# Kernel tuning notes

Measured on AMD Instinct MI355X. Metric: run time of the kernel, lower is better.

Reference implementation:

```python
import jax, jax.numpy as jnp
import numpy as np

DIM_MODEL = 512
KDIM = 64
NUM_FREQS = 70


def setup_inputs() -> dict:
    key = jax.random.key(0)
    ks = jax.random.split(key, 8)
    B, N = 8, 2048
    src = jax.random.normal(ks[0], (B, N, DIM_MODEL), dtype=jnp.float32)
    bias_tensor = jax.random.normal(ks[1], (N, N, 4), dtype=jnp.float32)
    multiplier = jax.random.uniform(ks[2], (B, N, N), dtype=jnp.float32)
    # f_theta_lc params
    W_r = jax.random.normal(ks[3], (NUM_FREQS, 2), dtype=jnp.float32)  # std=1.0 init
    C = jnp.ones((NUM_FREQS,), dtype=jnp.float32)
    log_p = jnp.float32(0.0)
    # Xavier-uniform attention projections (torch Linear weight layout [out, in])
    lim = float(np.sqrt(6.0 / (DIM_MODEL + KDIM)))
    W_q = jax.random.uniform(ks[4], (KDIM, DIM_MODEL), minval=-lim, maxval=lim, dtype=jnp.float32)
    W_k = jax.random.uniform(ks[5], (KDIM, DIM_MODEL), minval=-lim, maxval=lim, dtype=jnp.float32)
    W_v = jax.random.uniform(ks[6], (KDIM, DIM_MODEL), minval=-lim, maxval=lim, dtype=jnp.float32)
    s = jnp.float32(1.0)
    return {"src": src, "bias_tensor": bias_tensor, "multiplier": multiplier,
            "W_r": W_r, "C": C, "log_p": log_p,
            "W_q": W_q, "W_k": W_k, "W_v": W_v, "s": s}


def _f_theta(bias_tensor, W_r, C, log_p):
    # bias_tensor: [N, N, 4]; W_r: [F, 2]
    k1 = jnp.einsum('nmi,fi->nmf', bias_tensor[:, :, 0:2], W_r)
    k2 = jnp.einsum('nmi,fi->nmf', bias_tensor[:, :, 2:4], W_r)
    diff = jnp.cos(k1) + jnp.sin(k1) - jnp.cos(k2) - jnp.sin(k2)
    sigma = jnp.abs(jnp.sum(diff * C, axis=-1))  # [N, N]
    p = jnp.clip(jnp.exp(log_p), 0.5, 3.0)
    return jnp.exp(-jnp.power(sigma + 1e-6, p))


def reference(src, bias_tensor, multiplier, W_r, C, log_p, W_q, W_k, W_v, s):
    B = _f_theta(bias_tensor, W_r, C, log_p)  # [N, N]
    Q = jnp.einsum('bnd,kd->bnk', src, W_q)
    K = jnp.einsum('bnd,kd->bnk', src, W_k)
    V = jnp.einsum('bnd,kd->bnk', src, W_v)
    denom = jnp.sqrt(jnp.float32(KDIM))
    logits = (jnp.einsum('bnk,bmk->bnm', Q, K) + B[None]) / denom
    logits = logits * (s * multiplier)
    attn = jax.nn.softmax(logits, axis=-1)
    return jnp.einsum('bnm,bmk->bnk', attn, V)
```

## Files before the change

### kernel.cpp

```cpp
#include <hip/hip_runtime.h>
#include <hip/hip_bf16.h>

#define N_SEQ 2048
#define NB 8
#define DM 512
#define KD 64
#define NF 70

#define TG 512
#define TRANGE 6.5f
#define TSCL (511.0f / 13.0f)
#define TOFS (6.5f * TSCL)

typedef float f32x4 __attribute__((ext_vector_type(4)));
typedef short v8s  __attribute__((ext_vector_type(8)));

__device__ __forceinline__ ushort f2bf(float x) {
    uint u = __float_as_uint(x);
    return (ushort)((u + 0x7FFFu + ((u >> 16) & 1u)) >> 16);
}
__device__ __forceinline__ float bf2f(ushort h) {
    return __uint_as_float(((uint)h) << 16);
}

__global__ __launch_bounds__(256) void tbuild_kernel(
    const float* __restrict__ Wr, const float* __restrict__ Cc,
    float* __restrict__ Tg)
{
    const float SQ2 = 1.41421356237309504880f;
    const float R2PI = 0.15915494309189533577f;
    int idx = blockIdx.x * 256 + threadIdx.x;
    int j = idx >> 9, i = idx & (TG - 1);
    const float h = 2.0f * TRANGE / (TG - 1);
    float y = -TRANGE + j * h;
    float x = -TRANGE + i * h;
    float g = 0.f;
    for (int f = 0; f < NF; ++f) {
        float w0 = Wr[2*f] * R2PI, w1 = Wr[2*f+1] * R2PI, cf = Cc[f];
        float k = __builtin_amdgcn_fractf(fmaf(x, w0, fmaf(y, w1, 0.125f)));
        g = fmaf(cf, __builtin_amdgcn_sinf(k), g);
    }
    Tg[idx] = g * SQ2;
}

__global__ __launch_bounds__(256) void tpack_kernel(
    const float* __restrict__ Tg, float4* __restrict__ T4)
{
    int idx = blockIdx.x * 256 + threadIdx.x;
    int j = idx >> 9, i = idx & (TG - 1);
    int i1 = min(i + 1, TG - 1);
    int j1 = min(j + 1, TG - 1);
    float4 q;
    q.x = Tg[j*TG + i];
    q.y = Tg[j*TG + i1];
    q.z = Tg[j1*TG + i];
    q.w = Tg[j1*TG + i1];
    T4[idx] = q;
}

__device__ __forceinline__ float tlookup(const float4* __restrict__ T4,
                                         float x, float y)
{
    float u = fmaf(x, TSCL, TOFS);
    float v = fmaf(y, TSCL, TOFS);
    u = fminf(fmaxf(u, 0.0f), 510.999f);
    v = fminf(fmaxf(v, 0.0f), 510.999f);
    int iu = (int)u, iv = (int)v;
    float fu = __builtin_amdgcn_fractf(u);
    float fv = __builtin_amdgcn_fractf(v);
    float4 q = T4[iv * TG + iu];
    float t0 = fmaf(fu, q.y - q.x, q.x);
    float t1 = fmaf(fu, q.w - q.z, q.z);
    return fmaf(fv, t1 - t0, t0);
}

__global__ __launch_bounds__(256) void ftheta_kernel(
    const float* __restrict__ bias, const float4* __restrict__ T4,
    const float* __restrict__ logp, ushort* __restrict__ Bm)
{
    int tid = threadIdx.x;
    long i0 = (long)blockIdx.x * 512 + tid;
    long i1 = i0 + 256;
    float4 a = ((const float4*)bias)[i0];
    float4 b = ((const float4*)bias)[i1];
    float gA1 = tlookup(T4, a.x, a.y);
    float gA2 = tlookup(T4, a.z, a.w);
    float gB1 = tlookup(T4, b.x, b.y);
    float gB2 = tlookup(T4, b.z, b.w);
    float s0 = fabsf(gA1 - gA2) + 1e-6f;
    float s1 = fabsf(gB1 - gB2) + 1e-6f;
    float p = __expf(logp[0]);
    p = fminf(fmaxf(p, 0.5f), 3.0f);
    if (p == 1.0f) {
        Bm[i0] = f2bf(__expf(-s0));
        Bm[i1] = f2bf(__expf(-s1));
    } else {
        Bm[i0] = f2bf(__expf(-__powf(s0, p)));
        Bm[i1] = f2bf(__expf(-__powf(s1, p)));
    }
}

__global__ __launch_bounds__(256) void qkv_kernel(
    const float* __restrict__ src, const float* __restrict__ Wq,
    const float* __restrict__ Wk, const float* __restrict__ Wv,
    ushort* __restrict__ Qh, ushort* __restrict__ Ql,
    ushort* __restrict__ Kh, ushort* __restrict__ VhT)
{
    __shared__ ushort sS[32][72];
    __shared__ ushort sW[192][72];
    int tid = threadIdx.x;
    int lane = tid & 63, w = tid >> 6;
    int wr = w >> 1, wc = w & 1;
    int g = lane >> 4, ln = lane & 15;
    int row0 = blockIdx.x * 32;

    f32x4 acc[6];
#pragma unroll
    for (int t = 0; t < 6; ++t) acc[t] = {0.f, 0.f, 0.f, 0.f};

    for (int kc = 0; kc < 8; ++kc) {
        int k0 = kc * 64;
        __syncthreads();
        {
            int r = tid >> 3, c8 = (tid & 7) * 8;
            float4 f0 = *(const float4*)&src[(long)(row0 + r)*DM + k0 + c8];
            float4 f1 = *(const float4*)&src[(long)(row0 + r)*DM + k0 + c8 + 4];
            *(ushort4*)&sS[r][c8] =
                make_ushort4(f2bf(f0.x), f2bf(f0.y), f2bf(f0.z), f2bf(f0.w));
            *(ushort4*)&sS[r][c8+4] =
                make_ushort4(f2bf(f1.x), f2bf(f1.y), f2bf(f1.z), f2bf(f1.w));
        }
        {
#pragma unroll
            for (int j = 0; j < 6; ++j) {
                int slot = tid + j*256;
                int r = slot >> 3, c8 = (slot & 7) * 8;
                const float* Wp = (r < 64) ? Wq : (r < 128 ? Wk : Wv);
                int rr = r & 63;
                float4 f0 = *(const float4*)&Wp[(long)rr*DM + k0 + c8];
                float4 f1 = *(const float4*)&Wp[(long)rr*DM + k0 + c8 + 4];
                *(ushort4*)&sW[r][c8] =
                    make_ushort4(f2bf(f0.x), f2bf(f0.y), f2bf(f0.z), f2bf(f0.w));
                *(ushort4*)&sW[r][c8+4] =
                    make_ushort4(f2bf(f1.x), f2bf(f1.y), f2bf(f1.z), f2bf(f1.w));
            }
        }
        __syncthreads();
#pragma unroll
        for (int kw = 0; kw < 2; ++kw) {
            v8s bsrc = *(const v8s*)&sS[16*wr + ln][32*kw + 8*g];
#pragma unroll
            for (int t = 0; t < 6; ++t) {
                v8s aw = *(const v8s*)&sW[96*wc + 16*t + ln][32*kw + 8*g];
                acc[t] = __builtin_amdgcn_mfma_f32_16x16x32_bf16(aw, bsrc, acc[t], 0, 0, 0);
            }
        }
    }
    int n = row0 + 16*wr + ln;
    int bb = n >> 11, nn = n & 2047;
#pragma unroll
    for (int t = 0; t < 6; ++t) {
        int c0 = 96*wc + 16*t + 4*g;
        f32x4 v = acc[t];
        ushort4 h = make_ushort4(f2bf(v[0]), f2bf(v[1]), f2bf(v[2]), f2bf(v[3]));
        if (c0 < 64) {
            *(ushort4*)&Qh[(long)n*KD + c0] = h;
            *(ushort4*)&Ql[(long)n*KD + c0] =
                make_ushort4(f2bf(v[0] - bf2f(h.x)), f2bf(v[1] - bf2f(h.y)),
                             f2bf(v[2] - bf2f(h.z)), f2bf(v[3] - bf2f(h.w)));
        } else if (c0 < 128) {
            *(ushort4*)&Kh[(long)n*KD + (c0 - 64)] = h;
        } else {
            int kv = c0 - 128;
            VhT[((long)bb*KD + kv + 0)*N_SEQ + nn] = h.x;
            VhT[((long)bb*KD + kv + 1)*N_SEQ + nn] = h.y;
            VhT[((long)bb*KD + kv + 2)*N_SEQ + nn] = h.z;
            VhT[((long)bb*KD + kv + 3)*N_SEQ + nn] = h.w;
        }
    }
}

__global__ __launch_bounds__(256, 4) void attn_mfma_kernel(
    const ushort* __restrict__ Qh, const ushort* __restrict__ Ql,
    const ushort* __restrict__ Kh, const ushort* __restrict__ VhT,
    const ushort* __restrict__ Bm, const float* __restrict__ mult,
    const float* __restrict__ sp,
    ushort* __restrict__ Opart, float* __restrict__ Mp, float* __restrict__ Lp)
{
    __shared__ ushort sKh[64][72];
    __shared__ ushort sVT[64][72];
    __shared__ ushort sP[4][16][72];

    int tid = threadIdx.x;
    int lane = tid & 63, w = tid >> 6;
    int g = lane >> 4, ln = lane & 15;
    int bid = blockIdx.x;
    int b = bid & 7, rest = bid >> 3, p = rest & 3, nt = rest >> 2;
    int n0 = nt * 64;

    int qrow = n0 + w*16 + ln;
    long qoff = ((long)b*N_SEQ + qrow)*KD + 8*g;
    v8s qh0 = *(const v8s*)&Qh[qoff];
    v8s qh1 = *(const v8s*)&Qh[qoff + 32];
    v8s ql0 = *(const v8s*)&Ql[qoff];
    v8s ql1 = *(const v8s*)&Ql[qoff + 32];

    float s  = sp[0];
    float qs = 0.125f * s;
    float M = -1e30f, L = 0.f;
    f32x4 accO[4];
#pragma unroll
    for (int i = 0; i < 4; ++i) accO[i] = {0.f, 0.f, 0.f, 0.f};

    long brow = (long)qrow * N_SEQ;
    long urow = ((long)b*N_SEQ + qrow) * N_SEQ;
    long vtb  = (long)b*KD*N_SEQ;
    long kbB  = (long)b*N_SEQ*KD;

    int srow = tid >> 3, sc8 = (tid & 7) * 8;

    uint4 rKh0, rKh1, rVT0, rVT1;
    ushort4 nBq[4]; float4 nUq[4];
    {
        int m0 = p*512;
        rKh0 = *(const uint4*)&Kh[kbB + (long)(m0+srow)*KD + sc8];
        rKh1 = *(const uint4*)&Kh[kbB + (long)(m0+srow+32)*KD + sc8];
        rVT0 = *(const uint4*)&VhT[vtb + (long)srow*N_SEQ + m0 + sc8];
        rVT1 = *(const uint4*)&VhT[vtb + (long)(srow+32)*N_SEQ + m0 + sc8];
#pragma unroll
        for (int sub = 0; sub < 4; ++sub) {
            nBq[sub] = *(const ushort4*)&Bm[brow + m0 + 16*sub + 4*g];
            nUq[sub] = *(const float4*)&mult[urow + m0 + 16*sub + 4*g];
        }
    }

    for (int mt = 0; mt < 8; ++mt) {
        int m0 = p*512 + mt*64;
        __syncthreads();
        *(uint4*)&sKh[srow][sc8]      = rKh0;
        *(uint4*)&sKh[srow + 32][sc8] = rKh1;
        *(uint4*)&sVT[srow][sc8]      = rVT0;
        *(uint4*)&sVT[srow + 32][sc8] = rVT1;
        __syncthreads();

        if (mt < 7) {
            int m1 = m0 + 64;
            rKh0 = *(const uint4*)&Kh[kbB + (long)(m1+srow)*KD + sc8];
            rKh1 = *(const uint4*)&Kh[kbB + (long)(m1+srow+32)*KD + sc8];
            rVT0 = *(const uint4*)&VhT[vtb + (long)srow*N_SEQ + m1 + sc8];
            rVT1 = *(const uint4*)&VhT[vtb + (long)(srow+32)*N_SEQ + m1 + sc8];
        }

        f32x4 S[4];
#pragma unroll
        for (int i = 0; i < 4; ++i) S[i] = {0.f, 0.f, 0.f, 0.f};
        __builtin_amdgcn_s_setprio(1);
#pragma unroll
        for (int ks = 0; ks < 2; ++ks) {
            v8s qh = ks ? qh1 : qh0;
            v8s ql = ks ? ql1 : ql0;
#pragma unroll
            for (int sub = 0; sub < 4; ++sub) {
                v8s kh = *(const v8s*)&sKh[16*sub + ln][32*ks + 8*g];
                S[sub] = __builtin_amdgcn_mfma_f32_16x16x32_bf16(kh, qh, S[sub], 0, 0, 0);
                S[sub] = __builtin_amdgcn_mfma_f32_16x16x32_bf16(kh, ql, S[sub], 0, 0, 0);
            }
        }
        __builtin_amdgcn_s_setprio(0);

        float lg[16]; float mx = -1e30f;
#pragma unroll
        for (int sub = 0; sub < 4; ++sub) {
            float b0 = bf2f(nBq[sub].x), b1 = bf2f(nBq[sub].y);
            float b2 = bf2f(nBq[sub].z), b3 = bf2f(nBq[sub].w);
            lg[4*sub+0] = (S[sub][0] + b0) * nUq[sub].x * qs;
            lg[4*sub+1] = (S[sub][1] + b1) * nUq[sub].y * qs;
            lg[4*sub+2] = (S[sub][2] + b2) * nUq[sub].z * qs;
            lg[4*sub+3] = (S[sub][3] + b3) * nUq[sub].w * qs;
            mx = fmaxf(mx, fmaxf(fmaxf(lg[4*sub+0], lg[4*sub+1]),
                                 fmaxf(lg[4*sub+2], lg[4*sub+3])));
        }
        if (mt < 7) {
            int m1 = m0 + 64;
#pragma unroll
            for (int sub = 0; sub < 4; ++sub) {
                nBq[sub] = *(const ushort4*)&Bm[brow + m1 + 16*sub + 4*g];
                nUq[sub] = *(const float4*)&mult[urow + m1 + 16*sub + 4*g];
            }
        }
        mx = fmaxf(mx, __shfl_xor(mx, 16));
        mx = fmaxf(mx, __shfl_xor(mx, 32));
        float Mn = fmaxf(M, mx);
        float sc = __expf(M - Mn);
        float ps = 0.f;
#pragma unroll
        for (int i = 0; i < 16; ++i) {
            float e = __expf(lg[i] - Mn);
            lg[i] = e; ps += e;
        }
        ps += __shfl_xor(ps, 16);
        ps += __shfl_xor(ps, 32);
        L = L * sc + ps; M = Mn;

#pragma unroll
        for (int sub = 0; sub < 4; ++sub)
            *(ushort4*)&sP[w][ln][16*sub + 4*g] =
                make_ushort4(f2bf(lg[4*sub+0]), f2bf(lg[4*sub+1]),
                             f2bf(lg[4*sub+2]), f2bf(lg[4*sub+3]));

#pragma unroll
        for (int i = 0; i < 4; ++i) accO[i] *= sc;
        __builtin_amdgcn_s_setprio(1);
#pragma unroll
        for (int ks = 0; ks < 2; ++ks) {
            v8s pp = *(const v8s*)&sP[w][ln][32*ks + 8*g];
#pragma unroll
            for (int sub = 0; sub < 4; ++sub) {
                v8s vh = *(const v8s*)&sVT[16*sub + ln][32*ks + 8*g];
                accO[sub] = __builtin_amdgcn_mfma_f32_16x16x32_bf16(vh, pp, accO[sub], 0, 0, 0);
            }
        }
        __builtin_amdgcn_s_setprio(0);
    }

    long ob = ((long)bid*64 + (w*16 + ln)) * 64;
#pragma unroll
    for (int sub = 0; sub < 4; ++sub)
        *(ushort4*)&Opart[ob + 16*sub + 4*g] =
            make_ushort4(f2bf(accO[sub][0]), f2bf(accO[sub][1]),
                         f2bf(accO[sub][2]), f2bf(accO[sub][3]));
    if (g == 0) {
        Mp[bid*64 + w*16 + ln] = M;
        Lp[bid*64 + w*16 + ln] = L;
    }
}

__global__ __launch_bounds__(256) void combine_kernel(
    const ushort* __restrict__ Opart, const float* __restrict__ Mp,
    const float* __restrict__ Lp, float* __restrict__ out)
{
    int idx = blockIdx.x * 256 + threadIdx.x;
    int kq = idx & 15;
    int row = idx >> 4;
    int b = row >> 11, n = row & 2047;
    int nt = n >> 6, r = n & 63;
    int bid0 = ((nt*4) << 3) | b;
    float Mq[4], Lq[4];
#pragma unroll
    for (int p = 0; p < 4; ++p) {
        Mq[p] = Mp[(bid0 + 8*p)*64 + r];
        Lq[p] = Lp[(bid0 + 8*p)*64 + r];
    }
    float Mx = fmaxf(fmaxf(Mq[0], Mq[1]), fmaxf(Mq[2], Mq[3]));
    float4 acc = make_float4(0.f, 0.f, 0.f, 0.f);
    float Ls = 0.f;
#pragma unroll
    for (int p = 0; p < 4; ++p) {
        float e = __expf(Mq[p] - Mx);
        Ls += Lq[p] * e;
        ushort4 o = *(const ushort4*)&Opart[((long)(bid0 + 8*p)*64 + r)*64 + 4*kq];
        acc.x = fmaf(e, bf2f(o.x), acc.x);
        acc.y = fmaf(e, bf2f(o.y), acc.y);
        acc.z = fmaf(e, bf2f(o.z), acc.z);
        acc.w = fmaf(e, bf2f(o.w), acc.w);
    }
    float inv = 1.0f / Ls;
    float4 o;
    o.x = acc.x * inv; o.y = acc.y * inv;
    o.z = acc.z * inv; o.w = acc.w * inv;
    *(float4*)&out[(long)row*64 + 4*kq] = o;
}

extern "C" void kernel_launch(void* const* d_in, const int* in_sizes, int n_in,
                              void* d_out, int out_size, void* d_ws, size_t ws_size,
                              hipStream_t stream) {
    const float* src  = (const float*)d_in[0];
    const float* bias = (const float*)d_in[1];
    const float* mult = (const float*)d_in[2];
    const float* Wr   = (const float*)d_in[3];
    const float* Cc   = (const float*)d_in[4];
    const float* logp = (const float*)d_in[5];
    const float* Wq   = (const float*)d_in[6];
    const float* Wk   = (const float*)d_in[7];
    const float* Wv   = (const float*)d_in[8];
    const float* sp   = (const float*)d_in[9];
    float* outp = (float*)d_out;

    const size_t QKV_E = (size_t)NB * N_SEQ * KD;
    ushort* wsu = (ushort*)d_ws;
    ushort* Bm  = wsu;
    ushort* Qh  = wsu + (size_t)N_SEQ * N_SEQ;
    ushort* Ql  = Qh + QKV_E;
    ushort* Kh  = Ql + QKV_E;
    ushort* VhT = Kh + QKV_E;
    ushort* Opart = VhT + QKV_E;
    float* Mp = (float*)(Opart + (size_t)1024 * 64 * 64);
    float* Lp = Mp + (size_t)1024 * 64;
    float4* T4 = (float4*)(Lp + (size_t)1024 * 64);
    float*  Tg = (float*)(T4 + (size_t)TG * TG);

    tbuild_kernel<<<(TG*TG)/256, 256, 0, stream>>>(Wr, Cc, Tg);
    tpack_kernel<<<(TG*TG)/256, 256, 0, stream>>>(Tg, T4);
    ftheta_kernel<<<(N_SEQ*(long)N_SEQ)/512, 256, 0, stream>>>(bias, T4, logp, Bm);
    qkv_kernel<<<(NB*N_SEQ)/32, 256, 0, stream>>>(src, Wq, Wk, Wv, Qh, Ql, Kh, VhT);
    attn_mfma_kernel<<<1024, 256, 0, stream>>>(Qh, Ql, Kh, VhT, Bm, mult, sp,
                                               Opart, Mp, Lp);
    combine_kernel<<<1024, 256, 0, stream>>>(Opart, Mp, Lp, outp);
}
```

Before: 126.9 us.

## Load K and V MFMA fragments directly from global, drop LDS staging

Removes the shared-memory staging of K and V tiles and their two block-wide barriers per tile. Each wave now loads its MFMA fragments straight from global memory into registers, and launch bounds drop to 3 blocks per SM. The aim is to remove barrier stalls and LDS traffic. The cost is that all four waves redundantly fetch the same K/V data through cache. Register pressure also rises, and the loads are no longer prefetched a tile ahead, so their latency may be exposed.

```diff
diff --git a/kernel.cpp b/kernel.cpp
--- a/kernel.cpp
+++ b/kernel.cpp
@@ -180,15 +180,13 @@
     }
 }
 
-__global__ __launch_bounds__(256, 4) void attn_mfma_kernel(
+__global__ __launch_bounds__(256, 3) void attn_mfma_kernel(
     const ushort* __restrict__ Qh, const ushort* __restrict__ Ql,
     const ushort* __restrict__ Kh, const ushort* __restrict__ VhT,
     const ushort* __restrict__ Bm, const float* __restrict__ mult,
     const float* __restrict__ sp,
     ushort* __restrict__ Opart, float* __restrict__ Mp, float* __restrict__ Lp)
 {
-    __shared__ ushort sKh[64][72];
-    __shared__ ushort sVT[64][72];
     __shared__ ushort sP[4][16][72];
 
     int tid = threadIdx.x;
@@ -214,19 +212,12 @@
 
     long brow = (long)qrow * N_SEQ;
     long urow = ((long)b*N_SEQ + qrow) * N_SEQ;
-    long vtb  = (long)b*KD*N_SEQ;
-    long kbB  = (long)b*N_SEQ*KD;
-
-    int srow = tid >> 3, sc8 = (tid & 7) * 8;
-
-    uint4 rKh0, rKh1, rVT0, rVT1;
+    long kfrag = (long)b*N_SEQ*KD + (long)ln*KD + 8*g;
+    long vfrag = (long)b*KD*N_SEQ + (long)ln*N_SEQ + 8*g;
+
     ushort4 nBq[4]; float4 nUq[4];
     {
         int m0 = p*512;
-        rKh0 = *(const uint4*)&Kh[kbB + (long)(m0+srow)*KD + sc8];
-        rKh1 = *(const uint4*)&Kh[kbB + (long)(m0+srow+32)*KD + sc8];
-        rVT0 = *(const uint4*)&VhT[vtb + (long)srow*N_SEQ + m0 + sc8];
-        rVT1 = *(const uint4*)&VhT[vtb + (long)(srow+32)*N_SEQ + m0 + sc8];
 #pragma unroll
         for (int sub = 0; sub < 4; ++sub) {
             nBq[sub] = *(const ushort4*)&Bm[brow + m0 + 16*sub + 4*g];
@@ -236,20 +227,13 @@
 
     for (int mt = 0; mt < 8; ++mt) {
         int m0 = p*512 + mt*64;
-        __syncthreads();
-        *(uint4*)&sKh[srow][sc8]      = rKh0;
-        *(uint4*)&sKh[srow + 32][sc8] = rKh1;
-        *(uint4*)&sVT[srow][sc8]      = rVT0;
-        *(uint4*)&sVT[srow + 32][sc8] = rVT1;
-        __syncthreads();
-
-        if (mt < 7) {
-            int m1 = m0 + 64;
-            rKh0 = *(const uint4*)&Kh[kbB + (long)(m1+srow)*KD + sc8];
-            rKh1 = *(const uint4*)&Kh[kbB + (long)(m1+srow+32)*KD + sc8];
-            rVT0 = *(const uint4*)&VhT[vtb + (long)srow*N_SEQ + m1 + sc8];
-            rVT1 = *(const uint4*)&VhT[vtb + (long)(srow+32)*N_SEQ + m1 + sc8];
-        }
+
+        v8s kh[2][4];
+#pragma unroll
+        for (int ks = 0; ks < 2; ++ks)
+#pragma unroll
+            for (int sub = 0; sub < 4; ++sub)
+                kh[ks][sub] = *(const v8s*)&Kh[kfrag + (long)(m0 + 16*sub)*KD + 32*ks];
 
         f32x4 S[4];
 #pragma unroll
@@ -261,12 +245,18 @@
             v8s ql = ks ? ql1 : ql0;
 #pragma unroll
             for (int sub = 0; sub < 4; ++sub) {
-                v8s kh = *(const v8s*)&sKh[16*sub + ln][32*ks + 8*g];
-                S[sub] = __builtin_amdgcn_mfma_f32_16x16x32_bf16(kh, qh, S[sub], 0, 0, 0);
-                S[sub] = __builtin_amdgcn_mfma_f32_16x16x32_bf16(kh, ql, S[sub], 0, 0, 0);
+                S[sub] = __builtin_amdgcn_mfma_f32_16x16x32_bf16(kh[ks][sub], qh, S[sub], 0, 0, 0);
+                S[sub] = __builtin_amdgcn_mfma_f32_16x16x32_bf16(kh[ks][sub], ql, S[sub], 0, 0, 0);
             }
         }
         __builtin_amdgcn_s_setprio(0);
+
+        v8s vh[2][4];
+#pragma unroll
+        for (int ks = 0; ks < 2; ++ks)
+#pragma unroll
+            for (int sub = 0; sub < 4; ++sub)
+                vh[ks][sub] = *(const v8s*)&VhT[vfrag + (long)(16*sub)*N_SEQ + m0 + 32*ks];
 
         float lg[16]; float mx = -1e30f;
 #pragma unroll
@@ -315,10 +305,8 @@
         for (int ks = 0; ks < 2; ++ks) {
             v8s pp = *(const v8s*)&sP[w][ln][32*ks + 8*g];
 #pragma unroll
-            for (int sub = 0; sub < 4; ++sub) {
-                v8s vh = *(const v8s*)&sVT[16*sub + ln][32*ks + 8*g];
-                accO[sub] = __builtin_amdgcn_mfma_f32_16x16x32_bf16(vh, pp, accO[sub], 0, 0, 0);
-            }
+            for (int sub = 0; sub < 4; ++sub)
+                accO[sub] = __builtin_amdgcn_mfma_f32_16x16x32_bf16(vh[ks][sub], pp, accO[sub], 0, 0, 0);
         }
         __builtin_amdgcn_s_setprio(0);
     }
```

Measured after the change: 172.7 us. 1.36x slower.
